# Kernel optimization log

Measured on AMD Instinct MI355X. Metric: run time of the kernel, lower is better.

Reference implementation:

```python
import jax, jax.numpy as jnp
import numpy as np
import math

B, S, HID, H, WBAND = 2, 4096, 768, 12, 128
D = HID // H  # 64


def _band_qk(q, k, w):
    """q,k: [B,S,H,D] -> banded scores [B,S,H,2w+1] (offset d -> key pos i+d-w)."""
    b, s, h, d = q.shape
    nc = s // w
    kp = jnp.pad(k, ((0, 0), (w, w), (0, 0), (0, 0)))  # zero padding_value
    idx = (jnp.arange(nc) * w)[:, None] + jnp.arange(3 * w)[None, :]  # [nc,3w]
    kw = kp[:, idx]                                   # [B,nc,3w,H,D]
    qc = q.reshape(b, nc, w, h, d)
    scores = jnp.einsum('bcxhd,bcyhd->bchxy', qc, kw)  # [B,nc,H,w,3w]
    # extract diagonals: P[x,dd] = scores[x, x+dd] via flatten/skew trick
    flat = scores.reshape(b, nc, h, w * 3 * w)
    flat = jnp.pad(flat, ((0, 0), (0, 0), (0, 0), (0, w)))
    diag = flat.reshape(b, nc, h, w, 3 * w + 1)[..., : 2 * w + 1]
    return diag.transpose(0, 1, 3, 2, 4).reshape(b, s, h, 2 * w + 1)


def _band_pv(p, v, w):
    """p: [B,S,H,2w+1], v: [B,S,H,D] -> context [B,S,H,D]."""
    b, s, h, k = p.shape
    d = v.shape[-1]
    nc = s // w
    vp = jnp.pad(v, ((0, 0), (w, w), (0, 0), (0, 0)))
    idx = (jnp.arange(nc) * w)[:, None] + jnp.arange(3 * w)[None, :]
    vw = vp[:, idx]                                   # [B,nc,3w,H,D]
    pc = p.reshape(b, nc, w, h, k).transpose(0, 1, 3, 2, 4)  # [B,nc,H,w,2w+1]
    pc = jnp.pad(pc, ((0, 0), (0, 0), (0, 0), (0, 0), (0, w)))  # [..,w,3w+1]
    band = pc.reshape(b, nc, h, w * (3 * w + 1))[..., : w * 3 * w]
    band = band.reshape(b, nc, h, w, 3 * w)           # M[x, x+dd] = p[x,dd]
    ctx = jnp.einsum('bchxy,bcyhd->bcxhd', band, vw)  # [B,nc,w,H,D]
    return ctx.reshape(b, s, h, d)


def setup_inputs() -> dict:
    key = jax.random.key(0)
    ks = jax.random.split(key, 8)
    init = lambda k, shp: (jax.random.normal(k, shp, jnp.float32) * 0.02)
    return {
        'x': jax.random.normal(ks[0], (B, S, HID), jnp.float32),
        'Wq': init(ks[1], (HID, HID)), 'bq': jnp.zeros((HID,), jnp.float32),
        'Wk': init(ks[2], (HID, HID)), 'bk': jnp.zeros((HID,), jnp.float32),
        'Wv': init(ks[3], (HID, HID)), 'bv': jnp.zeros((HID,), jnp.float32),
        'Wd': init(ks[4], (H, D, HID)), 'bd': jnp.zeros((HID,), jnp.float32),
        'gamma': jnp.ones((HID,), jnp.float32),
        'beta': jnp.zeros((HID,), jnp.float32),
    }


def reference(x, Wq, bq, Wk, bk, Wv, bv, Wd, bd, gamma, beta):
    w = WBAND
    b, s, _ = x.shape
    q = (x @ Wq + bq).reshape(b, s, H, D) / math.sqrt(D)
    k = (x @ Wk + bk).reshape(b, s, H, D)
    v = (x @ Wv + bv).reshape(b, s, H, D)
    scores = _band_qk(q, k, w)                        # [B,S,H,2w+1]
    # mask_invalid_locations: key pos i + d - w must lie in [0, S)
    pos = jnp.arange(s)[:, None] + jnp.arange(2 * w + 1)[None, :] - w
    valid = (pos >= 0) & (pos < s)                    # [S,2w+1]
    scores = jnp.where(valid[None, :, None, :], scores, -1e9)
    probs = jax.nn.softmax(scores, axis=-1)           # float32 softmax
    ctx = _band_pv(probs, v, w)                       # [B,S,H,D]
    proj = jnp.einsum('bfnd,ndh->bfh', ctx, Wd) + bd  # output projection
    y = x + proj                                      # residual (dropout=0)
    mu = jnp.mean(y, axis=-1, keepdims=True)
    var = jnp.mean(jnp.square(y - mu), axis=-1, keepdims=True)
    out = (y - mu) / jnp.sqrt(var + 1e-12) * gamma + beta
    return out
```

## Files before the change

kernel.cpp:

```cpp
#include <hip/hip_runtime.h>
#include <math.h>

typedef unsigned short u16;
typedef __bf16 bf16x8 __attribute__((ext_vector_type(8)));
typedef float f32x4 __attribute__((ext_vector_type(4)));

constexpr int Bc   = 2;
constexpr int Sc   = 4096;
constexpr int HIDc = 768;
constexpr int Hc   = 12;
constexpr int Dc   = 64;
constexpr int Wc   = 128;
constexpr int Mc   = Bc * Sc;

constexpr int QT2  = 64;
constexpr int WIN  = QT2 + 2 * Wc;
constexpr int NCT  = WIN / 16;

static __device__ __forceinline__ void load_lds16(const void* g, void* l) {
    __builtin_amdgcn_global_load_lds(
        (const __attribute__((address_space(1))) void*)g,
        (__attribute__((address_space(3))) void*)l, 16, 0, 0);
}
static __device__ __forceinline__ u16 to_bf16(float f) {
    return __builtin_bit_cast(u16, (__bf16)f);
}

__global__ __launch_bounds__(256) void prep_x(const float* __restrict__ x,
                                              u16* __restrict__ xb,
                                              u16* __restrict__ zpad)
{
    int i = blockIdx.x * 256 + threadIdx.x;
    float4 v = ((const float4*)x)[i];
    ushort4 o;
    o.x = to_bf16(v.x); o.y = to_bf16(v.y);
    o.z = to_bf16(v.z); o.w = to_bf16(v.w);
    ((ushort4*)xb)[i] = o;
    if (blockIdx.x == 0 && threadIdx.x < 128)
        ((int4*)zpad)[threadIdx.x] = make_int4(0, 0, 0, 0);
}

__global__ __launch_bounds__(256) void prep_w(
    const float* __restrict__ Wq, const float* __restrict__ Wk,
    const float* __restrict__ Wv, const float* __restrict__ Wd,
    u16* __restrict__ wqt, u16* __restrict__ wkt,
    u16* __restrict__ wvt, u16* __restrict__ wdt)
{
    const int z = blockIdx.z;
    const float* W = z == 0 ? Wq : z == 1 ? Wk : z == 2 ? Wv : Wd;
    u16* T         = z == 0 ? wqt : z == 1 ? wkt : z == 2 ? wvt : wdt;

    __shared__ float t[32][33];
    const int bx = blockIdx.x * 32, by = blockIdx.y * 32;
    const int tx = threadIdx.x & 31, ty = threadIdx.x >> 5;
#pragma unroll
    for (int i = 0; i < 32; i += 8)
        t[ty + i][tx] = W[(size_t)(by + ty + i) * HIDc + bx + tx];
    __syncthreads();
#pragma unroll
    for (int i = 0; i < 32; i += 8)
        T[(size_t)(bx + ty + i) * HIDc + by + tx] = to_bf16(t[tx][ty + i]);
}

__device__ __forceinline__ void stage_tile(const u16* __restrict__ M,
                                           int r0, int k0, u16* lds)
{
    const int tid = threadIdx.x;
#pragma unroll
    for (int i = 0; i < 2; ++i) {
        int u    = tid + i * 256;
        int pair = u >> 3, phys = u & 7;
        int s8   = phys ^ (pair & 7);
        int row  = 2 * pair + (s8 >> 2);
        int kseg = s8 & 3;
        load_lds16(M + (size_t)(r0 + row) * HIDc + k0 + kseg * 8,
                   (char*)lds + u * 16);
    }
}

template <int SWAP>
__device__ __forceinline__ void gemm128_core(
    const u16* __restrict__ A, const u16* __restrict__ Bt,
    int m0, int n0, u16* As, u16* Bs, f32x4 (&acc)[4][4])
{
    const int lane = threadIdx.x & 63, wid = threadIdx.x >> 6;
    const int c16 = lane & 15, g = lane >> 4;
    const int wm = (wid >> 1) * 64, wn = (wid & 1) * 64;

    stage_tile(A,  m0, 0, As);
    stage_tile(Bt, n0, 0, Bs);
    __syncthreads();
    int cur = 0;
    for (int t = 0; t < 24; ++t) {
        if (t + 1 < 24) {
            stage_tile(A,  m0, (t + 1) * 32, As + (cur ^ 1) * 4096);
            stage_tile(Bt, n0, (t + 1) * 32, Bs + (cur ^ 1) * 4096);
        }
        bf16x8 af[4], bfr[4];
#pragma unroll
        for (int tt = 0; tt < 4; ++tt) {
            int ar = wm + tt * 16 + c16;
            int ap = ar >> 1, a8 = (((ar & 1) << 2) | g) ^ (ap & 7);
            af[tt] = *(const bf16x8*)(As + cur * 4096 + ap * 64 + a8 * 8);
            int br = wn + tt * 16 + c16;
            int bp = br >> 1, b8 = (((br & 1) << 2) | g) ^ (bp & 7);
            bfr[tt] = *(const bf16x8*)(Bs + cur * 4096 + bp * 64 + b8 * 8);
        }
        __builtin_amdgcn_s_setprio(1);
#pragma unroll
        for (int mt = 0; mt < 4; ++mt)
#pragma unroll
            for (int nt = 0; nt < 4; ++nt)
                acc[mt][nt] = SWAP
                    ? __builtin_amdgcn_mfma_f32_16x16x32_bf16(
                          bfr[nt], af[mt], acc[mt][nt], 0, 0, 0)
                    : __builtin_amdgcn_mfma_f32_16x16x32_bf16(
                          af[mt], bfr[nt], acc[mt][nt], 0, 0, 0);
        __builtin_amdgcn_s_setprio(0);
        __syncthreads();
        cur ^= 1;
    }
}

__global__ __launch_bounds__(256) void gemm_qk_mfma(
    const u16* __restrict__ xb,
    const u16* __restrict__ wqt, const u16* __restrict__ wkt,
    const float* __restrict__ bq, const float* __restrict__ bk,
    u16* __restrict__ qg, u16* __restrict__ kg)
{
    __shared__ u16 As[8192], Bs[8192];
    const int z = blockIdx.z;
    const u16* Bt     = z ? wkt : wqt;
    const float* bias = z ? bk : bq;
    const float scale = z ? 1.0f : 0.125f;
    u16* outp         = z ? kg : qg;

    const int m0 = blockIdx.x * 128, n0 = blockIdx.y * 128;
    f32x4 acc[4][4];
#pragma unroll
    for (int i = 0; i < 4; ++i)
#pragma unroll
        for (int j = 0; j < 4; ++j) acc[i][j] = (f32x4){0.f, 0.f, 0.f, 0.f};

    gemm128_core<1>(xb, Bt, m0, n0, As, Bs, acc);

    const int lane = threadIdx.x & 63, wid = threadIdx.x >> 6;
    const int c16 = lane & 15, g = lane >> 4;
    const int wm = (wid >> 1) * 64, wn = (wid & 1) * 64;

#pragma unroll
    for (int mt = 0; mt < 4; ++mt) {
        int m = m0 + wm + mt * 16 + c16;
        int b = m >> 12, s = m & (Sc - 1);
        size_t rowbase = (size_t)(b * Hc) * Sc * Dc + (size_t)s * Dc;
#pragma unroll
        for (int nt = 0; nt < 4; ++nt) {
            int nb = n0 + wn + nt * 16 + g * 4;
            int h = nb >> 6, d0 = nb & 63;
            float4 b4 = *(const float4*)&bias[nb];
            ushort4 pk;
            pk.x = to_bf16((acc[mt][nt][0] + b4.x) * scale);
            pk.y = to_bf16((acc[mt][nt][1] + b4.y) * scale);
            pk.z = to_bf16((acc[mt][nt][2] + b4.z) * scale);
            pk.w = to_bf16((acc[mt][nt][3] + b4.w) * scale);
            *(ushort4*)&outp[rowbase + (size_t)h * Sc * Dc + d0] = pk;
        }
    }
}

__global__ __launch_bounds__(256) void gemm_v_mfma(
    const u16* __restrict__ xb, const u16* __restrict__ wvt,
    const float* __restrict__ bv, u16* __restrict__ vtg)
{
    __shared__ u16 As[8192], Bs[8192];
    const int m0 = blockIdx.x * 128, n0 = blockIdx.y * 128;
    f32x4 acc[4][4];
#pragma unroll
    for (int i = 0; i < 4; ++i)
#pragma unroll
        for (int j = 0; j < 4; ++j) acc[i][j] = (f32x4){0.f, 0.f, 0.f, 0.f};

    gemm128_core<0>(xb, wvt, m0, n0, As, Bs, acc);

    const int lane = threadIdx.x & 63, wid = threadIdx.x >> 6;
    const int c16 = lane & 15, g = lane >> 4;
    const int wm = (wid >> 1) * 64, wn = (wid & 1) * 64;

#pragma unroll
    for (int nt = 0; nt < 4; ++nt) {
        int n = n0 + wn + nt * 16 + c16;
        int h = n >> 6, d = n & 63;
        float bn = bv[n];
#pragma unroll
        for (int mt = 0; mt < 4; ++mt) {
            int m = m0 + wm + mt * 16 + g * 4;
            int b = m >> 12, s = m & (Sc - 1);
            size_t base = ((size_t)(b * Hc + h)) * Sc * Dc + (size_t)d * Sc + s;
            ushort4 pk;
            pk.x = to_bf16(acc[mt][nt][0] + bn);
            pk.y = to_bf16(acc[mt][nt][1] + bn);
            pk.z = to_bf16(acc[mt][nt][2] + bn);
            pk.w = to_bf16(acc[mt][nt][3] + bn);
            *(ushort4*)&vtg[base] = pk;
        }
    }
}

__global__ __launch_bounds__(256) void gemm_proj_mfma(
    const u16* __restrict__ ctxb, const u16* __restrict__ wdt,
    const float* __restrict__ bd, const float* __restrict__ x,
    float* __restrict__ y)
{
    __shared__ u16 As[8192], Bs[8192];
    const int m0 = blockIdx.x * 128, n0 = blockIdx.y * 128;
    f32x4 acc[4][4];
#pragma unroll
    for (int i = 0; i < 4; ++i)
#pragma unroll
        for (int j = 0; j < 4; ++j) acc[i][j] = (f32x4){0.f, 0.f, 0.f, 0.f};

    gemm128_core<1>(ctxb, wdt, m0, n0, As, Bs, acc);

    const int lane = threadIdx.x & 63, wid = threadIdx.x >> 6;
    const int c16 = lane & 15, g = lane >> 4;
    const int wm = (wid >> 1) * 64, wn = (wid & 1) * 64;

#pragma unroll
    for (int mt = 0; mt < 4; ++mt) {
        int m = m0 + wm + mt * 16 + c16;
#pragma unroll
        for (int nt = 0; nt < 4; ++nt) {
            int nb = n0 + wn + nt * 16 + g * 4;
            float4 b4 = *(const float4*)&bd[nb];
            float4 x4 = *(const float4*)&x[(size_t)m * HIDc + nb];
            float4 o4;
            o4.x = acc[mt][nt][0] + b4.x + x4.x;
            o4.y = acc[mt][nt][1] + b4.y + x4.y;
            o4.z = acc[mt][nt][2] + b4.z + x4.z;
            o4.w = acc[mt][nt][3] + b4.w + x4.w;
            *(float4*)&y[(size_t)m * HIDc + nb] = o4;
        }
    }
}

__global__ __launch_bounds__(256) void band_attn_mfma(
    const u16* __restrict__ qg, const u16* __restrict__ kg,
    const u16* __restrict__ vtg, const u16* __restrict__ zpad,
    u16* __restrict__ ctxb)
{
    extern __shared__ u16 sm[];
    u16* kwin = sm;
    u16* vt   = sm + 20480;
    u16* pm   = sm;

    const int L = blockIdx.x;
    const int xcd = L & 7, tt = L >> 3;
    const int hb = xcd * 3 + (tt % 3);
    const int qc = tt / 3;
    const int h = hb % Hc, b = hb / Hc;

    const int s0 = qc * QT2;
    const int tid = threadIdx.x;
    const int lane = tid & 63, wid = tid >> 6;
    const int c16 = lane & 15, g = lane >> 4;
    const size_t hbase = ((size_t)(b * Hc + h)) * Sc * Dc;

#pragma unroll
    for (int i = 0; i < 10; ++i) {
        int c   = i * 4 + wid;
        int row = c * 8 + (lane >> 3);
        int seg = (lane & 7) ^ (lane >> 3);
        int pos = s0 - Wc + row;
        const u16* src = (pos >= 0 && pos < Sc)
                       ? &kg[hbase + (size_t)pos * Dc + seg * 8] : zpad;
        load_lds16(src, (char*)kwin + c * 1024 + (lane & 63) * 16);
    }
#pragma unroll
    for (int i = 0; i < 10; ++i) {
        int c   = i * 4 + wid;
        int idx = c * 64 + lane;
        int d   = idx / 40;
        int p   = idx - d * 40;
        int seg = (p & 0x38) | ((p ^ d) & 7);
        int pos0 = s0 - Wc + seg * 8;
        const u16* src = (pos0 >= 0 && pos0 < Sc)
                       ? &vtg[hbase + (size_t)d * Sc + pos0] : zpad;
        load_lds16(src, (char*)vt + idx * 16);
    }

    const u16* qp = &qg[hbase + (size_t)(s0 + wid * 16 + c16) * Dc + g * 8];
    bf16x8 qa0 = *(const bf16x8*)qp;
    bf16x8 qa1 = *(const bf16x8*)(qp + 32);

    __syncthreads();

    f32x4 acc[NCT];
#pragma unroll
    for (int ct = 0; ct < NCT; ++ct) acc[ct] = (f32x4){0.f, 0.f, 0.f, 0.f};
    __builtin_amdgcn_s_setprio(1);
#pragma unroll
    for (int ct = 0; ct < NCT; ++ct) {
        int row = ct * 16 + c16;
        const u16* kb = kwin + row * 64;
        bf16x8 kb0 = *(const bf16x8*)(kb + (g       ^ (row & 7)) * 8);
        bf16x8 kb1 = *(const bf16x8*)(kb + ((g + 4) ^ (row & 7)) * 8);
        acc[ct] = __builtin_amdgcn_mfma_f32_16x16x32_bf16(qa0, kb0, acc[ct], 0, 0, 0);
        acc[ct] = __builtin_amdgcn_mfma_f32_16x16x32_bf16(qa1, kb1, acc[ct], 0, 0, 0);
    }
    __builtin_amdgcn_s_setprio(0);

    float mrow[4] = {-3e38f, -3e38f, -3e38f, -3e38f};
#pragma unroll
    for (int ct = 0; ct < NCT; ++ct) {
#pragma unroll
        for (int r = 0; r < 4; ++r) {
            int rl  = wid * 16 + g * 4 + r;
            int j   = ct * 16 + c16;
            int pos = s0 - Wc + j;
            bool valid = (j >= rl) && (j <= rl + 2 * Wc) && (pos >= 0) && (pos < Sc);
            float v = valid ? acc[ct][r] : -3e38f;
            acc[ct][r] = v;
            mrow[r] = fmaxf(mrow[r], v);
        }
    }
#pragma unroll
    for (int r = 0; r < 4; ++r)
#pragma unroll
        for (int off = 1; off < 16; off <<= 1)
            mrow[r] = fmaxf(mrow[r], __shfl_xor(mrow[r], off));

    float srow[4] = {0.f, 0.f, 0.f, 0.f};
#pragma unroll
    for (int ct = 0; ct < NCT; ++ct)
#pragma unroll
        for (int r = 0; r < 4; ++r) {
            float e = __expf(acc[ct][r] - mrow[r]);
            acc[ct][r] = e;
            srow[r] += e;
        }
#pragma unroll
    for (int r = 0; r < 4; ++r)
#pragma unroll
        for (int off = 1; off < 16; off <<= 1)
            srow[r] += __shfl_xor(srow[r], off);

    __syncthreads();

#pragma unroll
    for (int ct = 0; ct < NCT; ++ct)
#pragma unroll
        for (int r = 0; r < 4; ++r) {
            int q   = wid * 16 + g * 4 + r;
            int col = ct * 16 + c16;
            int sl  = col >> 3;
            int ph  = (sl & 0x38) | ((sl ^ q ^ (q >> 3)) & 7);
            pm[q * 320 + ph * 8 + (col & 7)] = to_bf16(acc[ct][r]);
        }

    float sq0 = __shfl(srow[0], (c16 >> 2) << 4);
    float sq1 = __shfl(srow[1], (c16 >> 2) << 4);
    float sq2 = __shfl(srow[2], (c16 >> 2) << 4);
    float sq3 = __shfl(srow[3], (c16 >> 2) << 4);
    int rr = c16 & 3;
    float sq = rr == 0 ? sq0 : rr == 1 ? sq1 : rr == 2 ? sq2 : sq3;
    float invq = 1.f / sq;

    f32x4 o[4];
#pragma unroll
    for (int dt = 0; dt < 4; ++dt) o[dt] = (f32x4){0.f, 0.f, 0.f, 0.f};
    const int qrow = wid * 16 + c16;
    __builtin_amdgcn_s_setprio(1);
#pragma unroll
    for (int ks = 0; ks < 10; ++ks) {
        int sl = ks * 4 + g;
        int ph = (sl & 0x38) | ((sl ^ qrow ^ (qrow >> 3)) & 7);
        bf16x8 pa = *(const bf16x8*)(pm + qrow * 320 + ph * 8);
#pragma unroll
        for (int dt = 0; dt < 4; ++dt) {
            int d  = dt * 16 + c16;
            int pv = (sl & 0x38) | ((sl ^ d) & 7);
            bf16x8 vb = *(const bf16x8*)(vt + d * 320 + pv * 8);
            o[dt] = __builtin_amdgcn_mfma_f32_16x16x32_bf16(vb, pa, o[dt], 0, 0, 0);
        }
    }
    __builtin_amdgcn_s_setprio(0);

    const size_t crow = ((size_t)(b * Sc + s0 + wid * 16 + c16)) * HIDc + h * Dc;
#pragma unroll
    for (int dt = 0; dt < 4; ++dt) {
        ushort4 pk;
        pk.x = to_bf16(o[dt][0] * invq);
        pk.y = to_bf16(o[dt][1] * invq);
        pk.z = to_bf16(o[dt][2] * invq);
        pk.w = to_bf16(o[dt][3] * invq);
        *(ushort4*)&ctxb[crow + dt * 16 + g * 4] = pk;
    }
}

__global__ __launch_bounds__(256) void ln_kernel(
    const float* __restrict__ y,
    const float* __restrict__ gamma, const float* __restrict__ beta,
    float* __restrict__ out)
{
    const int m = blockIdx.x;
    const float* row = y + (size_t)m * HIDc;
    const int t = threadIdx.x;
    float v0 = row[t], v1 = row[t + 256], v2 = row[t + 512];
    float s = v0 + v1 + v2;
    __shared__ float red[4];
    const int lane = t & 63, wid = t >> 6;
#pragma unroll
    for (int o = 1; o < 64; o <<= 1) s += __shfl_xor(s, o);
    if (lane == 0) red[wid] = s;
    __syncthreads();
    const float mu = (red[0] + red[1] + red[2] + red[3]) * (1.f / HIDc);
    v0 -= mu; v1 -= mu; v2 -= mu;
    float s2 = v0 * v0 + v1 * v1 + v2 * v2;
#pragma unroll
    for (int o = 1; o < 64; o <<= 1) s2 += __shfl_xor(s2, o);
    __syncthreads();
    if (lane == 0) red[wid] = s2;
    __syncthreads();
    const float var = (red[0] + red[1] + red[2] + red[3]) * (1.f / HIDc);
    const float rstd = rsqrtf(var + 1e-12f);
    const size_t base = (size_t)m * HIDc;
    out[base + t]       = v0 * rstd * gamma[t]       + beta[t];
    out[base + t + 256] = v1 * rstd * gamma[t + 256] + beta[t + 256];
    out[base + t + 512] = v2 * rstd * gamma[t + 512] + beta[t + 512];
}

extern "C" void kernel_launch(void* const* d_in, const int* in_sizes, int n_in,
                              void* d_out, int out_size, void* d_ws, size_t ws_size,
                              hipStream_t stream)
{
    const float* x     = (const float*)d_in[0];
    const float* Wq    = (const float*)d_in[1];
    const float* bq    = (const float*)d_in[2];
    const float* Wk    = (const float*)d_in[3];
    const float* bk    = (const float*)d_in[4];
    const float* Wv    = (const float*)d_in[5];
    const float* bv    = (const float*)d_in[6];
    const float* Wd    = (const float*)d_in[7];
    const float* bd    = (const float*)d_in[8];
    const float* gamma = (const float*)d_in[9];
    const float* beta  = (const float*)d_in[10];
    float* out = (float*)d_out;

    constexpr size_t CHUNK = (size_t)Mc * HIDc;
    constexpr size_t WSZ   = (size_t)HIDc * HIDc;
    u16* xb   = (u16*)d_ws;
    u16* wqt  = xb + CHUNK;
    u16* wkt  = wqt + WSZ;
    u16* wvt  = wkt + WSZ;
    u16* wdt  = wvt + WSZ;
    u16* qg   = wdt + WSZ;
    u16* kg   = qg + CHUNK;
    u16* vtg  = kg + CHUNK;
    u16* ctxb = vtg + CHUNK;
    float* yws = (float*)(ctxb + CHUNK);
    u16* zpad  = (u16*)(yws + CHUNK);

    prep_x<<<(CHUNK / 4) / 256, 256, 0, stream>>>(x, xb, zpad);
    prep_w<<<dim3(24, 24, 4), 256, 0, stream>>>(Wq, Wk, Wv, Wd, wqt, wkt, wvt, wdt);

    gemm_qk_mfma<<<dim3(Mc / 128, HIDc / 128, 2), 256, 0, stream>>>(
        xb, wqt, wkt, bq, bk, qg, kg);
    gemm_v_mfma<<<dim3(Mc / 128, HIDc / 128), 256, 0, stream>>>(
        xb, wvt, bv, vtg);

    band_attn_mfma<<<dim3(Sc / QT2 * Hc * Bc), 256, 81920, stream>>>(
        qg, kg, vtg, zpad, ctxb);

    gemm_proj_mfma<<<dim3(Mc / 128, HIDc / 128), 256, 0, stream>>>(
        ctxb, wdt, bd, x, yws);

    ln_kernel<<<Mc, 256, 0, stream>>>(yws, gamma, beta, out);
}
```

Baseline: 144.3 us.

## Deepen GEMM K-tile to 64 with partial vmcnt barriers and earlier Q loads

The shared GEMM core now stages 64-wide K tiles (12 iterations instead of 24) with a new row-major swizzled LDS layout, and doubles the LDS buffers. It replaces __syncthreads with a raw s_waitcnt vmcnt(N) plus s_barrier so the prefetch of the next tile stays in flight while the current one is consumed. The attention kernel issues its Q register loads before the K/V LDS loads and waits only on the older K loads before the QK^T step, deferring the V wait to the later barrier. This cuts barrier count and load stalls, at the cost of more LDS per block (possibly lower occupancy) and reliance on hand-counted vmcnt values, which break if the compiler reorders or adds memory ops.

```diff
diff --git a/kernel.cpp b/kernel.cpp
--- a/kernel.cpp
+++ b/kernel.cpp
@@ -16,6 +16,9 @@
 constexpr int QT2  = 64;
 constexpr int WIN  = QT2 + 2 * Wc;
 constexpr int NCT  = WIN / 16;
+
+#define VM_BAR(N) asm volatile("s_waitcnt vmcnt(" #N ")\n\ts_barrier" ::: "memory")
+#define BAR()     asm volatile("s_barrier" ::: "memory")
 
 static __device__ __forceinline__ void load_lds16(const void* g, void* l) {
     __builtin_amdgcn_global_load_lds(
@@ -62,19 +65,19 @@
         T[(size_t)(bx + ty + i) * HIDc + by + tx] = to_bf16(t[tx][ty + i]);
 }
 
-__device__ __forceinline__ void stage_tile(const u16* __restrict__ M,
-                                           int r0, int k0, u16* lds)
-{
-    const int tid = threadIdx.x;
-#pragma unroll
-    for (int i = 0; i < 2; ++i) {
-        int u    = tid + i * 256;
-        int pair = u >> 3, phys = u & 7;
-        int s8   = phys ^ (pair & 7);
-        int row  = 2 * pair + (s8 >> 2);
-        int kseg = s8 & 3;
-        load_lds16(M + (size_t)(r0 + row) * HIDc + k0 + kseg * 8,
-                   (char*)lds + u * 16);
+__device__ __forceinline__ void stage64(const u16* __restrict__ A,
+                                        const u16* __restrict__ Bt,
+                                        int m0, int n0, int k0,
+                                        u16* As, u16* Bs, int soff)
+{
+#pragma unroll
+    for (int i = 0; i < 4; ++i) {
+        int off  = soff + i * 1024;
+        int row  = off >> 7;
+        int slot = (off >> 4) & 7;
+        int seg  = slot ^ (row & 7);
+        load_lds16(A  + (size_t)(m0 + row) * HIDc + k0 + seg * 8, (char*)As + off);
+        load_lds16(Bt + (size_t)(n0 + row) * HIDc + k0 + seg * 8, (char*)Bs + off);
     }
 }
 
@@ -86,38 +89,45 @@
     const int lane = threadIdx.x & 63, wid = threadIdx.x >> 6;
     const int c16 = lane & 15, g = lane >> 4;
     const int wm = (wid >> 1) * 64, wn = (wid & 1) * 64;
-
-    stage_tile(A,  m0, 0, As);
-    stage_tile(Bt, n0, 0, Bs);
-    __syncthreads();
+    const int soff = wid * 4096 + lane * 16;
+
+    stage64(A, Bt, m0, n0, 0, As, Bs, soff);
     int cur = 0;
-    for (int t = 0; t < 24; ++t) {
-        if (t + 1 < 24) {
-            stage_tile(A,  m0, (t + 1) * 32, As + (cur ^ 1) * 4096);
-            stage_tile(Bt, n0, (t + 1) * 32, Bs + (cur ^ 1) * 4096);
-        }
-        bf16x8 af[4], bfr[4];
-#pragma unroll
-        for (int tt = 0; tt < 4; ++tt) {
-            int ar = wm + tt * 16 + c16;
-            int ap = ar >> 1, a8 = (((ar & 1) << 2) | g) ^ (ap & 7);
-            af[tt] = *(const bf16x8*)(As + cur * 4096 + ap * 64 + a8 * 8);
-            int br = wn + tt * 16 + c16;
-            int bp = br >> 1, b8 = (((br & 1) << 2) | g) ^ (bp & 7);
-            bfr[tt] = *(const bf16x8*)(Bs + cur * 4096 + bp * 64 + b8 * 8);
-        }
-        __builtin_amdgcn_s_setprio(1);
-#pragma unroll
-        for (int mt = 0; mt < 4; ++mt)
-#pragma unroll
-            for (int nt = 0; nt < 4; ++nt)
-                acc[mt][nt] = SWAP
-                    ? __builtin_amdgcn_mfma_f32_16x16x32_bf16(
-                          bfr[nt], af[mt], acc[mt][nt], 0, 0, 0)
-                    : __builtin_amdgcn_mfma_f32_16x16x32_bf16(
-                          af[mt], bfr[nt], acc[mt][nt], 0, 0, 0);
-        __builtin_amdgcn_s_setprio(0);
-        __syncthreads();
+    for (int t = 0; t < 12; ++t) {
+        if (t < 11) {
+            stage64(A, Bt, m0, n0, (t + 1) * 64,
+                    As + (cur ^ 1) * 8192, Bs + (cur ^ 1) * 8192, soff);
+            VM_BAR(8);
+        } else {
+            VM_BAR(0);
+        }
+        const u16* Ab = As + cur * 8192;
+        const u16* Bb = Bs + cur * 8192;
+#pragma unroll
+        for (int kk = 0; kk < 2; ++kk) {
+            bf16x8 af[4], bfr[4];
+#pragma unroll
+            for (int tt = 0; tt < 4; ++tt) {
+                int ar = wm + tt * 16 + c16;
+                int a8 = (kk * 4 + g) ^ (ar & 7);
+                af[tt] = *(const bf16x8*)(Ab + ar * 64 + a8 * 8);
+                int br = wn + tt * 16 + c16;
+                int b8 = (kk * 4 + g) ^ (br & 7);
+                bfr[tt] = *(const bf16x8*)(Bb + br * 64 + b8 * 8);
+            }
+            __builtin_amdgcn_s_setprio(1);
+#pragma unroll
+            for (int mt = 0; mt < 4; ++mt)
+#pragma unroll
+                for (int nt = 0; nt < 4; ++nt)
+                    acc[mt][nt] = SWAP
+                        ? __builtin_amdgcn_mfma_f32_16x16x32_bf16(
+                              bfr[nt], af[mt], acc[mt][nt], 0, 0, 0)
+                        : __builtin_amdgcn_mfma_f32_16x16x32_bf16(
+                              af[mt], bfr[nt], acc[mt][nt], 0, 0, 0);
+            __builtin_amdgcn_s_setprio(0);
+        }
+        BAR();
         cur ^= 1;
     }
 }
@@ -128,7 +138,7 @@
     const float* __restrict__ bq, const float* __restrict__ bk,
     u16* __restrict__ qg, u16* __restrict__ kg)
 {
-    __shared__ u16 As[8192], Bs[8192];
+    __shared__ u16 As[16384], Bs[16384];
     const int z = blockIdx.z;
     const u16* Bt     = z ? wkt : wqt;
     const float* bias = z ? bk : bq;
@@ -172,7 +182,7 @@
     const u16* __restrict__ xb, const u16* __restrict__ wvt,
     const float* __restrict__ bv, u16* __restrict__ vtg)
 {
-    __shared__ u16 As[8192], Bs[8192];
+    __shared__ u16 As[16384], Bs[16384];
     const int m0 = blockIdx.x * 128, n0 = blockIdx.y * 128;
     f32x4 acc[4][4];
 #pragma unroll
@@ -211,7 +221,7 @@
     const float* __restrict__ bd, const float* __restrict__ x,
     float* __restrict__ y)
 {
-    __shared__ u16 As[8192], Bs[8192];
+    __shared__ u16 As[16384], Bs[16384];
     const int m0 = blockIdx.x * 128, n0 = blockIdx.y * 128;
     f32x4 acc[4][4];
 #pragma unroll
@@ -265,6 +275,10 @@
     const int c16 = lane & 15, g = lane >> 4;
     const size_t hbase = ((size_t)(b * Hc + h)) * Sc * Dc;
 
+    const u16* qp = &qg[hbase + (size_t)(s0 + wid * 16 + c16) * Dc + g * 8];
+    bf16x8 qa0 = *(const bf16x8*)qp;
+    bf16x8 qa1 = *(const bf16x8*)(qp + 32);
+
 #pragma unroll
     for (int i = 0; i < 10; ++i) {
         int c   = i * 4 + wid;
@@ -288,11 +302,7 @@
         load_lds16(src, (char*)vt + idx * 16);
     }
 
-    const u16* qp = &qg[hbase + (size_t)(s0 + wid * 16 + c16) * Dc + g * 8];
-    bf16x8 qa0 = *(const bf16x8*)qp;
-    bf16x8 qa1 = *(const bf16x8*)(qp + 32);
-
-    __syncthreads();
+    VM_BAR(10);
 
     f32x4 acc[NCT];
 #pragma unroll
@@ -344,7 +354,7 @@
         for (int off = 1; off < 16; off <<= 1)
             srow[r] += __shfl_xor(srow[r], off);
 
-    __syncthreads();
+    VM_BAR(0);
 
 #pragma unroll
     for (int ct = 0; ct < NCT; ++ct)
```

Result: faster. 126.7 us (-12.2%).
